# Kernel tuning notes

Measured on AMD Instinct MI355X. Metric: run time of the kernel, lower is better.

Reference implementation:

```python
import jax, jax.numpy as jnp
import numpy as np

EPS = 1e-9
TOP_K = 2
CAPACITY_FACTOR = 4.0
MIN_EXPERT_CAPACITY = 4


def setup_inputs() -> dict:
    key = jax.random.key(0)
    k1, k2 = jax.random.split(key)
    x = jax.random.normal(k1, (4, 32, 512, 24, 24), dtype=jnp.float32)
    w_gating = jax.random.normal(k2, (512, 16), dtype=jnp.float32)
    return {"x": x, "w_gating": w_gating}


def cumsum_exclusive(t, axis):
    # exclusive cumsum along `axis`: cumsum shifted by one (zero first)
    return jnp.cumsum(t, axis=axis) - t


def reference(x, w_gating):
    T, B, D, H, W = x.shape
    N = H * W                       # group_size (tokens per image)
    E = w_gating.shape[1]           # num_gates / experts
    dt = x.dtype

    # pool over timesteps: (T,B,D,H,W) -> (B,N,D)
    x_tok = x.reshape(T, B, D, N).transpose(0, 1, 3, 2)
    x_pooled = x_tok.mean(axis=0)

    raw_gates = jax.nn.softmax(jnp.einsum('bnd,de->bne', x_pooled, w_gating), axis=-1)

    # --- top-k selection loop (importance=None, so no importance masking) ---
    gates_remaining = raw_gates
    masks, gates, indices = [], [], []
    for k in range(TOP_K):
        index_k = jnp.argmax(gates_remaining, axis=-1)                 # (B,N)
        gate_k = jnp.take_along_axis(gates_remaining, index_k[..., None], axis=-1)[..., 0]
        mask_k = jax.nn.one_hot(index_k, E, dtype=dt)                  # (B,N,E)
        masks.append(mask_k)
        gates.append(gate_k)
        indices.append(index_k)
        gates_remaining = gates_remaining * (1.0 - mask_k)

    gate_sum = sum(gates) + EPS
    gates = [g / gate_sum for g in gates]

    # load-balancing loss
    density_1 = masks[0].mean(axis=-2)          # (B,E)
    density_1_proxy = raw_gates.mean(axis=-2)   # (B,E)
    loss = (density_1_proxy * density_1).mean() * float(E ** 2)

    # policy == 'all': masks unchanged

    expert_capacity = min(N, int(N * CAPACITY_FACTOR / E))
    expert_capacity = max(expert_capacity, MIN_EXPERT_CAPACITY)
    cap_f = float(expert_capacity)

    # --- capacity assignment ---
    cumulative_position = jnp.zeros((B, 1, E), dtype=dt)
    positions = [None] * TOP_K
    for k in range(TOP_K):
        position_k = cumsum_exclusive(masks[k], axis=-2) + cumulative_position
        position_k = position_k * masks[k]
        masks[k] = masks[k] * (position_k < cap_f).astype(dt)
        positions[k] = position_k.sum(axis=-1)                          # (B,N)
        gates[k] = gates[k] * masks[k].sum(axis=-1)
        cumulative_position = cumulative_position + masks[k].sum(axis=-2, keepdims=True)

    # --- combine / dispatch tensors (B, N, E, C) ---
    combine_tensor = jnp.zeros((B, N, E, expert_capacity), dtype=dt)
    for k in range(TOP_K):
        mask_k_flat = masks[k].sum(axis=-1)                             # (B,N)
        expert_oh = jax.nn.one_hot(indices[k], E, dtype=dt)             # (B,N,E)
        # out-of-range positions produce all-zero rows, matching safe_one_hot's slice
        pos_oh = jax.nn.one_hot(positions[k].astype(jnp.int32), expert_capacity, dtype=dt)  # (B,N,C)
        combine_tensor = combine_tensor + (
            (gates[k] * mask_k_flat)[..., None, None]
            * expert_oh[..., None]
            * pos_oh[..., None, :]
        )
    dispatch_tensor = (combine_tensor != 0).astype(dt)
    return dispatch_tensor, combine_tensor, loss
```

## Files before the change

### kernel.cpp

```cpp
#include <hip/hip_runtime.h>

#define TT 4
#define BB 32
#define DD 512
#define NN 576
#define EE 16
#define CC 144
#define DC 8
#define DCH 64
#define ROW (EE*CC)
#define SZ 42467328UL

__global__ __launch_bounds__(576) void k_part(const float* __restrict__ x,
                                              const float* __restrict__ w,
                                              float* __restrict__ part) {
  const int b  = blockIdx.x;
  const int dc = blockIdx.y;
  const int n  = threadIdx.x;
  const int d0 = dc * DCH;

  float acc[EE];
#pragma unroll
  for (int e = 0; e < EE; ++e) acc[e] = 0.f;

  for (int t = 0; t < TT; ++t) {
    const float* xp = x + (((size_t)t * BB + b) * DD + d0) * NN + n;
    for (int dd = 0; dd < DCH; dd += 8) {
      float xv[8];
#pragma unroll
      for (int u = 0; u < 8; ++u) xv[u] = xp[(size_t)(dd + u) * NN];
#pragma unroll
      for (int u = 0; u < 8; ++u) {
        const float* wd = w + (size_t)(d0 + dd + u) * EE;
#pragma unroll
        for (int e = 0; e < EE; ++e) acc[e] = fmaf(xv[u], wd[e], acc[e]);
      }
    }
  }

  float4* dst4 = (float4*)(part + (((size_t)b * NN + n) * DC + dc) * EE);
#pragma unroll
  for (int q = 0; q < 4; ++q)
    dst4[q] = make_float4(acc[4*q], acc[4*q+1], acc[4*q+2], acc[4*q+3]);
}

__global__ __launch_bounds__(576) void k_gate(const float* __restrict__ part,
                                              float4* __restrict__ info,
                                              float* __restrict__ lossp) {
  const int b = blockIdx.x;
  const int n = threadIdx.x;
  const int wave = n >> 6, lane = n & 63;

  __shared__ float sprox[9][EE];
  __shared__ int   swc1[9][EE];
  __shared__ int   swc2[9][EE];
  __shared__ int   woff1[9][EE];
  __shared__ int   woff2[9][EE];
  __shared__ float sproxTot[EE];
  __shared__ int   scnt0[EE];
  __shared__ int   sbase2[EE];

  float l[EE];
#pragma unroll
  for (int e = 0; e < EE; ++e) l[e] = 0.f;
  {
    const float4* p4 = (const float4*)(part + (size_t)(b * NN + n) * (DC * EE));
#pragma unroll
    for (int dc = 0; dc < DC; ++dc) {
#pragma unroll
      for (int q = 0; q < 4; ++q) {
        float4 v = p4[dc * 4 + q];
        l[4*q+0] += v.x; l[4*q+1] += v.y; l[4*q+2] += v.z; l[4*q+3] += v.w;
      }
    }
#pragma unroll
    for (int e = 0; e < EE; ++e) l[e] *= 0.25f;
  }

  float m = l[0];
#pragma unroll
  for (int e = 1; e < EE; ++e) m = fmaxf(m, l[e]);
  float raw[EE]; float s = 0.f;
#pragma unroll
  for (int e = 0; e < EE; ++e) { raw[e] = expf(l[e] - m); s += raw[e]; }
  float inv = 1.f / s;
#pragma unroll
  for (int e = 0; e < EE; ++e) raw[e] *= inv;

  int e1 = 0; float g1 = raw[0];
#pragma unroll
  for (int e = 1; e < EE; ++e) if (raw[e] > g1) { g1 = raw[e]; e1 = e; }
  int e2 = (e1 == 0) ? 1 : 0; float g2 = raw[e2];
#pragma unroll
  for (int e = 0; e < EE; ++e) if (e != e1 && raw[e] > g2) { g2 = raw[e]; e2 = e; }
  const float denom = g1 + g2 + 1e-9f;
  const float w0 = g1 / denom, w1 = g2 / denom;

  const unsigned long long ltm = (1ull << lane) - 1ull;
  int pre1 = 0, pre2 = 0;
#pragma unroll
  for (int e = 0; e < EE; ++e) {
    unsigned long long m1 = __ballot(e1 == e);
    unsigned long long m2 = __ballot(e2 == e);
    if (lane == 0) { swc1[wave][e] = __popcll(m1); swc2[wave][e] = __popcll(m2); }
    if (e == e1) pre1 = __popcll(m1 & ltm);
    if (e == e2) pre2 = __popcll(m2 & ltm);
  }

#pragma unroll
  for (int e = 0; e < EE; ++e) {
    float v = raw[e];
#pragma unroll
    for (int off = 32; off; off >>= 1) v += __shfl_xor(v, off);
    if (lane == 0) sprox[wave][e] = v;
  }
  __syncthreads();

  if (n < EE) {
    int r1 = 0, r2 = 0; float pv = 0.f;
#pragma unroll
    for (int wv = 0; wv < 9; ++wv) {
      woff1[wv][n] = r1; r1 += swc1[wv][n];
      woff2[wv][n] = r2; r2 += swc2[wv][n];
      pv += sprox[wv][n];
    }
    scnt0[n]    = r1;
    sbase2[n]   = r1 < CC ? r1 : CC;
    sproxTot[n] = pv;
  }
  __syncthreads();

  if (n == 0) {
    float S = 0.f;
    for (int e = 0; e < EE; ++e) S += sproxTot[e] * (float)scnt0[e];
    lossp[b] = S / ((float)NN * (float)NN);
  }

  const int p0 = woff1[wave][e1] + pre1;
  const int p1 = sbase2[e2] + woff2[wave][e2] + pre2;

  const int  pos0 = (p0 < CC) ? (e1 * CC + p0) : -1;
  const int  pos1 = (p1 < CC) ? (e2 * CC + p1) : -1;
  const float w0k = (p0 < CC) ? w0 : 0.f;
  const float w1k = (p1 < CC) ? w1 : 0.f;

  float4 o;
  o.x = __int_as_float(pos0);
  o.y = w0k;
  o.z = __int_as_float(pos1);
  o.w = w1k;
  info[b * NN + n] = o;
}

__global__ __launch_bounds__(192) void k_write(const float4* __restrict__ info,
                                               const float* __restrict__ lossp,
                                               float* __restrict__ out) {
  const int tok = blockIdx.x;
  if (tok == 0 && threadIdx.x == 0) {
    float sv = 0.f;
    for (int b = 0; b < BB; ++b) sv += lossp[b];
    out[2 * SZ] = 0.5f * sv;
  }
  const float4 inf = info[tok];
  const int   pos0 = __float_as_int(inf.x);
  const float w0   = inf.y;
  const int   pos1 = __float_as_int(inf.z);
  const float w1   = inf.w;

  float4* disp = (float4*)(out + (size_t)tok * ROW);
  float4* comb = (float4*)(out + SZ + (size_t)tok * ROW);

#pragma unroll
  for (int it = 0; it < 3; ++it) {
    const int i  = threadIdx.x + it * 192;
    const int f0 = i * 4;
    float c0 = (f0+0 == pos0) ? w0 : ((f0+0 == pos1) ? w1 : 0.f);
    float c1 = (f0+1 == pos0) ? w0 : ((f0+1 == pos1) ? w1 : 0.f);
    float c2 = (f0+2 == pos0) ? w0 : ((f0+2 == pos1) ? w1 : 0.f);
    float c3 = (f0+3 == pos0) ? w0 : ((f0+3 == pos1) ? w1 : 0.f);
    float d0 = (c0 != 0.f) ? 1.f : 0.f;
    float d1 = (c1 != 0.f) ? 1.f : 0.f;
    float d2 = (c2 != 0.f) ? 1.f : 0.f;
    float d3 = (c3 != 0.f) ? 1.f : 0.f;
    comb[i] = make_float4(c0, c1, c2, c3);
    disp[i] = make_float4(d0, d1, d2, d3);
  }
}

extern "C" void kernel_launch(void* const* d_in, const int* in_sizes, int n_in,
                              void* d_out, int out_size, void* d_ws, size_t ws_size,
                              hipStream_t stream) {
  const float* x = (const float*)d_in[0];
  const float* w = (const float*)d_in[1];
  float* out = (float*)d_out;

  float*  part  = (float*)d_ws;
  float4* info  = (float4*)((char*)d_ws + 9437184);
  float*  lossp = (float*)((char*)d_ws + 9437184 + 294912);

  hipLaunchKernelGGL(k_part,  dim3(BB, DC), dim3(576), 0, stream, x, w, part);
  hipLaunchKernelGGL(k_gate,  dim3(BB),     dim3(576), 0, stream, part, info, lossp);
  hipLaunchKernelGGL(k_write, dim3(BB*NN),  dim3(192), 0, stream, info, lossp, out);
}
```

Measured before the change: 123.8 us.

## Fuse output zero-fill into pooling kernel and scatter nonzeros separately

```diff
diff --git a/kernel.cpp b/kernel.cpp
--- a/kernel.cpp
+++ b/kernel.cpp
@@ -5,20 +5,29 @@
 #define DD 512
 #define NN 576
 #define EE 16
-#define CC 144
 #define DC 8
 #define DCH 64
+#define CC 144
 #define ROW (EE*CC)
 #define SZ 42467328UL
-
-__global__ __launch_bounds__(576) void k_part(const float* __restrict__ x,
-                                              const float* __restrict__ w,
-                                              float* __restrict__ part) {
+#define Z4PB 82944
+#define Z4PT 144
+
+typedef float f4 __attribute__((ext_vector_type(4)));
+
+__global__ __launch_bounds__(576) void k_partzero(const float* __restrict__ x,
+                                                  const float* __restrict__ w,
+                                                  float* __restrict__ part,
+                                                  float* __restrict__ out) {
   const int b  = blockIdx.x;
   const int dc = blockIdx.y;
   const int n  = threadIdx.x;
   const int d0 = dc * DCH;
 
+  f4* outz = (f4*)out;
+  const size_t zbase = (size_t)(b + dc * BB) * Z4PB + n;
+  const f4 zv = {0.f, 0.f, 0.f, 0.f};
+
   float acc[EE];
 #pragma unroll
   for (int e = 0; e < EE; ++e) acc[e] = 0.f;
@@ -36,6 +45,9 @@
         for (int e = 0; e < EE; ++e) acc[e] = fmaf(xv[u], wd[e], acc[e]);
       }
     }
+#pragma unroll 4
+    for (int k = t * 36; k < t * 36 + 36; ++k)
+      outz[zbase + (size_t)k * 576] = zv;
   }
 
   float4* dst4 = (float4*)(part + (((size_t)b * NN + n) * DC + dc) * EE);
@@ -152,39 +164,23 @@
   info[b * NN + n] = o;
 }
 
-__global__ __launch_bounds__(192) void k_write(const float4* __restrict__ info,
-                                               const float* __restrict__ lossp,
-                                               float* __restrict__ out) {
-  const int tok = blockIdx.x;
-  if (tok == 0 && threadIdx.x == 0) {
+__global__ __launch_bounds__(512) void k_scatter(const float4* __restrict__ info,
+                                                 const float* __restrict__ lossp,
+                                                 float* __restrict__ out) {
+  const int tok = blockIdx.x * 512 + threadIdx.x;
+  if (tok == 0) {
     float sv = 0.f;
     for (int b = 0; b < BB; ++b) sv += lossp[b];
     out[2 * SZ] = 0.5f * sv;
   }
   const float4 inf = info[tok];
   const int   pos0 = __float_as_int(inf.x);
-  const float w0   = inf.y;
   const int   pos1 = __float_as_int(inf.z);
-  const float w1   = inf.w;
-
-  float4* disp = (float4*)(out + (size_t)tok * ROW);
-  float4* comb = (float4*)(out + SZ + (size_t)tok * ROW);
-
-#pragma unroll
-  for (int it = 0; it < 3; ++it) {
-    const int i  = threadIdx.x + it * 192;
-    const int f0 = i * 4;
-    float c0 = (f0+0 == pos0) ? w0 : ((f0+0 == pos1) ? w1 : 0.f);
-    float c1 = (f0+1 == pos0) ? w0 : ((f0+1 == pos1) ? w1 : 0.f);
-    float c2 = (f0+2 == pos0) ? w0 : ((f0+2 == pos1) ? w1 : 0.f);
-    float c3 = (f0+3 == pos0) ? w0 : ((f0+3 == pos1) ? w1 : 0.f);
-    float d0 = (c0 != 0.f) ? 1.f : 0.f;
-    float d1 = (c1 != 0.f) ? 1.f : 0.f;
-    float d2 = (c2 != 0.f) ? 1.f : 0.f;
-    float d3 = (c3 != 0.f) ? 1.f : 0.f;
-    comb[i] = make_float4(c0, c1, c2, c3);
-    disp[i] = make_float4(d0, d1, d2, d3);
-  }
+
+  float* disp = out + (size_t)tok * ROW;
+  float* comb = out + SZ + (size_t)tok * ROW;
+  if (pos0 >= 0) { disp[pos0] = 1.f; comb[pos0] = inf.y; }
+  if (pos1 >= 0) { disp[pos1] = 1.f; comb[pos1] = inf.w; }
 }
 
 extern "C" void kernel_launch(void* const* d_in, const int* in_sizes, int n_in,
@@ -198,7 +194,7 @@
   float4* info  = (float4*)((char*)d_ws + 9437184);
   float*  lossp = (float*)((char*)d_ws + 9437184 + 294912);
 
-  hipLaunchKernelGGL(k_part,  dim3(BB, DC), dim3(576), 0, stream, x, w, part);
-  hipLaunchKernelGGL(k_gate,  dim3(BB),     dim3(576), 0, stream, part, info, lossp);
-  hipLaunchKernelGGL(k_write, dim3(BB*NN),  dim3(192), 0, stream, info, lossp, out);
-}
+  hipLaunchKernelGGL(k_partzero, dim3(BB, DC), dim3(576), 0, stream, x, w, part, out);
+  hipLaunchKernelGGL(k_gate,     dim3(BB),     dim3(576), 0, stream, part, info, lossp);
+  hipLaunchKernelGGL(k_scatter,  dim3(36),     dim3(512), 0, stream, info, lossp, out);
+}
```

New measurement: 138.0 us. +11.5%, slower.
